# Kernel optimization log

Measured on AMD Instinct MI355X. Metric: run time of the kernel, lower is better.

## Reference

```python
import jax, jax.numpy as jnp
import numpy as np

INPUT_DIM = 256
OUTPUT_DIM = 512
NUM_KNOTS = 64
RANGE_KNOTS = (-1.0, 1.0)
DEGREE = 3
BATCH = 4096


def bspline_basis(x, knots, degree):
    """Cox-de Boor recursion. x: [B, I], knots: [K] (uniform, ascending).
    Returns basis values [B, I, K - degree - 1]."""
    xe = x[..., None]  # [B, I, 1]
    # degree-0: indicator of knot interval k, k = 0..K-2
    basis = ((xe >= knots[:-1]) & (xe < knots[1:])).astype(x.dtype)  # [B, I, K-1]
    for d in range(1, degree + 1):
        k = np.arange(knots.shape[0] - d - 1)
        left = (xe - knots[k]) / (knots[k + d] - knots[k]) * basis[..., :-1]
        right = (knots[k + d + 1] - xe) / (knots[k + d + 1] - knots[k + 1]) * basis[..., 1:]
        basis = left + right  # [B, I, K-d-1]
    return basis


def setup_inputs() -> dict:
    key = jax.random.key(0)
    kx, kb, ks = jax.random.split(key, 3)
    x = jax.random.uniform(kx, (BATCH, INPUT_DIM), dtype=jnp.float32)
    wb = jax.random.uniform(kb, (INPUT_DIM, OUTPUT_DIM), dtype=jnp.float32)
    ws = jax.random.uniform(ks, (INPUT_DIM, OUTPUT_DIM), dtype=jnp.float32)
    cps = jnp.ones((INPUT_DIM, NUM_KNOTS), dtype=jnp.float32)
    knots = jnp.asarray(np.linspace(RANGE_KNOTS[0], RANGE_KNOTS[1], NUM_KNOTS), dtype=jnp.float32)
    return {"x": x, "wb": wb, "ws": ws, "cps": cps, "knots": knots}


def reference(x, wb, ws, cps, knots):
    num_basis = NUM_KNOTS - DEGREE - 1
    basis = bspline_basis(x, knots, DEGREE)            # [B, I, num_basis]
    # per-input-dim spline value: sum_k cps[i, k] * B_k(x[b, i])
    spline = jnp.einsum('bik,ik->bi', basis, cps[:, :num_basis])  # [B, I]
    base = jax.nn.silu(x)                               # [B, I]
    # out[b, o] = sum_i wb[i, o] * silu(x[b, i]) + ws[i, o] * spline[b, i]
    out = base @ wb + spline @ ws                       # [B, O]
    return out
```

## Files before the change

kernel.cpp:

```cpp
#include <hip/hip_runtime.h>
#include <hip/hip_bf16.h>

#define BATCH    4096
#define IN_DIM   256
#define OUT_DIM  512
#define KDIM     512
#define NKNOTS   64
#define NBASIS   60

typedef __attribute__((ext_vector_type(8))) short bf16x8;
typedef __attribute__((ext_vector_type(4))) float f32x4;

__device__ __forceinline__ short f2bf(float f) {
    __hip_bfloat16 h = __float2bfloat16(f);
    return *reinterpret_cast<short*>(&h);
}

__global__ __launch_bounds__(256) void prep_a_kernel(
        const float* __restrict__ x, const float* __restrict__ cps,
        const float* __restrict__ knots, short* __restrict__ A) {
    int idx = blockIdx.x * 256 + threadIdx.x;
    int b = idx >> 8;
    int i = idx & (IN_DIM - 1);

    float xv = x[idx];
    float base = xv / (1.0f + __expf(-xv));

    float u = (xv + 1.0f) * 31.5f;
    int   j = (int)floorf(u);
    float spline = 0.0f;
    if (j >= 0 && j <= 62) {
        float t  = (xv - knots[j]) * 31.5f;
        float t2 = t * t, t3 = t2 * t;
        float omt = 1.0f - t;
        const float c6 = 1.0f / 6.0f;
        float w0 = omt * omt * omt * c6;
        float w1 = (3.0f*t3 - 6.0f*t2 + 4.0f) * c6;
        float w2 = (-3.0f*t3 + 3.0f*t2 + 3.0f*t + 1.0f) * c6;
        float w3 = t3 * c6;
        const float* cp = cps + i * NKNOTS;
        int k0 = j - 3;
        if (k0     >= 0 && k0     < NBASIS) spline += w0 * cp[k0];
        if (k0 + 1 >= 0 && k0 + 1 < NBASIS) spline += w1 * cp[k0 + 1];
        if (k0 + 2 >= 0 && k0 + 2 < NBASIS) spline += w2 * cp[k0 + 2];
        if (k0 + 3 >= 0 && k0 + 3 < NBASIS) spline += w3 * cp[k0 + 3];
    }

    A[b * KDIM + i]          = f2bf(base);
    A[b * KDIM + IN_DIM + i] = f2bf(spline);
}

__global__ __launch_bounds__(256) void prep_b_kernel(
        const float* __restrict__ wb, const float* __restrict__ ws,
        short* __restrict__ Bt) {
    int idx = blockIdx.x * 256 + threadIdx.x;
    int n = idx >> 9;
    int k = idx & (KDIM - 1);
    float v = (k < IN_DIM) ? wb[k * OUT_DIM + n] : ws[(k - IN_DIM) * OUT_DIM + n];
    Bt[idx] = f2bf(v);
}

#define BM 64
#define BN 64
#define BK 64
#define LDSS 72

__global__ __launch_bounds__(256) void gemm_kernel(
        const short* __restrict__ A, const short* __restrict__ Bt,
        float* __restrict__ C) {
    __shared__ __align__(16) short As[BM * LDSS];
    __shared__ __align__(16) short Bs[BN * LDSS];

    const int m0 = blockIdx.y * BM;
    const int n0 = blockIdx.x * BN;
    const int tid  = threadIdx.x;
    const int lane = tid & 63;
    const int wave = tid >> 6;
    const int wm = (wave & 1) * 32;
    const int wn = (wave >> 1) * 32;
    const int fr   = lane & 15;
    const int koff = (lane >> 4) * 8;

    f32x4 acc[2][2] = {};

    const int c1 = tid, c2 = tid + 256;
    const int r1 = c1 >> 3, o1 = (c1 & 7) * 8;
    const int r2 = c2 >> 3, o2 = (c2 & 7) * 8;

    for (int k0 = 0; k0 < KDIM; k0 += BK) {
        *(uint4*)&As[r1 * LDSS + o1] = *(const uint4*)&A[(m0 + r1) * KDIM + k0 + o1];
        *(uint4*)&As[r2 * LDSS + o2] = *(const uint4*)&A[(m0 + r2) * KDIM + k0 + o2];
        *(uint4*)&Bs[r1 * LDSS + o1] = *(const uint4*)&Bt[(n0 + r1) * KDIM + k0 + o1];
        *(uint4*)&Bs[r2 * LDSS + o2] = *(const uint4*)&Bt[(n0 + r2) * KDIM + k0 + o2];
        __syncthreads();

        #pragma unroll
        for (int kk = 0; kk < BK; kk += 32) {
            bf16x8 a0 = *(const bf16x8*)&As[(wm + fr)      * LDSS + kk + koff];
            bf16x8 a1 = *(const bf16x8*)&As[(wm + 16 + fr) * LDSS + kk + koff];
            bf16x8 b0 = *(const bf16x8*)&Bs[(wn + fr)      * LDSS + kk + koff];
            bf16x8 b1 = *(const bf16x8*)&Bs[(wn + 16 + fr) * LDSS + kk + koff];
            acc[0][0] = __builtin_amdgcn_mfma_f32_16x16x32_bf16(a0, b0, acc[0][0], 0, 0, 0);
            acc[0][1] = __builtin_amdgcn_mfma_f32_16x16x32_bf16(a0, b1, acc[0][1], 0, 0, 0);
            acc[1][0] = __builtin_amdgcn_mfma_f32_16x16x32_bf16(a1, b0, acc[1][0], 0, 0, 0);
            acc[1][1] = __builtin_amdgcn_mfma_f32_16x16x32_bf16(a1, b1, acc[1][1], 0, 0, 0);
        }
        __syncthreads();
    }

    const int rbase = (lane >> 4) * 4;
    #pragma unroll
    for (int mt = 0; mt < 2; ++mt) {
        #pragma unroll
        for (int nt = 0; nt < 2; ++nt) {
            #pragma unroll
            for (int r = 0; r < 4; ++r) {
                int row = m0 + wm + mt * 16 + rbase + r;
                int col = n0 + wn + nt * 16 + fr;
                C[row * OUT_DIM + col] = acc[mt][nt][r];
            }
        }
    }
}

extern "C" void kernel_launch(void* const* d_in, const int* in_sizes, int n_in,
                              void* d_out, int out_size, void* d_ws, size_t ws_size,
                              hipStream_t stream) {
    const float* x     = (const float*)d_in[0];
    const float* wb    = (const float*)d_in[1];
    const float* ws    = (const float*)d_in[2];
    const float* cps   = (const float*)d_in[3];
    const float* knots = (const float*)d_in[4];
    float* out = (float*)d_out;

    short* Abf = (short*)d_ws;
    short* Btb = (short*)((char*)d_ws + (size_t)BATCH * KDIM * 2);

    prep_a_kernel<<<BATCH * IN_DIM / 256, 256, 0, stream>>>(x, cps, knots, Abf);
    prep_b_kernel<<<OUT_DIM * KDIM / 256, 256, 0, stream>>>(wb, ws, Btb);

    dim3 grid(OUT_DIM / BN, BATCH / BM);
    gemm_kernel<<<grid, 256, 0, stream>>>(Abf, Btb, out);
}
```

Baseline: 84.39 us.

## Fuse prep kernels, tile-transpose weights, use direct global-to-LDS loads with XOR swizzle

Merges the two prep kernels into one launch. Activation blocks stage a transposed bf16 copy of the control points in LDS, and weight blocks transpose through a padded LDS tile so both reads and writes are coalesced. The GEMM now uses global_load_lds to write tiles straight into LDS, with an XOR swizzle in place of padding to avoid bank conflicts. The control points are rounded to bf16 before use, which adds a small precision loss, and the prep kernel now launches only 320 blocks.

New measurement: 84.81 us, median of 2. Within noise of the previous version (+0.5%).

```diff
diff --git a/kernel.cpp b/kernel.cpp
--- a/kernel.cpp
+++ b/kernel.cpp
@@ -15,91 +15,129 @@
     __hip_bfloat16 h = __float2bfloat16(f);
     return *reinterpret_cast<short*>(&h);
 }
-
-__global__ __launch_bounds__(256) void prep_a_kernel(
-        const float* __restrict__ x, const float* __restrict__ cps,
-        const float* __restrict__ knots, short* __restrict__ A) {
-    int idx = blockIdx.x * 256 + threadIdx.x;
-    int b = idx >> 8;
-    int i = idx & (IN_DIM - 1);
-
-    float xv = x[idx];
-    float base = xv / (1.0f + __expf(-xv));
-
-    float u = (xv + 1.0f) * 31.5f;
-    int   j = (int)floorf(u);
-    float spline = 0.0f;
-    if (j >= 0 && j <= 62) {
-        float t  = (xv - knots[j]) * 31.5f;
-        float t2 = t * t, t3 = t2 * t;
-        float omt = 1.0f - t;
-        const float c6 = 1.0f / 6.0f;
-        float w0 = omt * omt * omt * c6;
-        float w1 = (3.0f*t3 - 6.0f*t2 + 4.0f) * c6;
-        float w2 = (-3.0f*t3 + 3.0f*t2 + 3.0f*t + 1.0f) * c6;
-        float w3 = t3 * c6;
-        const float* cp = cps + i * NKNOTS;
-        int k0 = j - 3;
-        if (k0     >= 0 && k0     < NBASIS) spline += w0 * cp[k0];
-        if (k0 + 1 >= 0 && k0 + 1 < NBASIS) spline += w1 * cp[k0 + 1];
-        if (k0 + 2 >= 0 && k0 + 2 < NBASIS) spline += w2 * cp[k0 + 2];
-        if (k0 + 3 >= 0 && k0 + 3 < NBASIS) spline += w3 * cp[k0 + 3];
-    }
-
-    A[b * KDIM + i]          = f2bf(base);
-    A[b * KDIM + IN_DIM + i] = f2bf(spline);
+__device__ __forceinline__ float bf2f(short s) {
+    __hip_bfloat16 h = *reinterpret_cast<__hip_bfloat16*>(&s);
+    return __bfloat162float(h);
 }
 
-__global__ __launch_bounds__(256) void prep_b_kernel(
-        const float* __restrict__ wb, const float* __restrict__ ws,
-        short* __restrict__ Bt) {
-    int idx = blockIdx.x * 256 + threadIdx.x;
-    int n = idx >> 9;
-    int k = idx & (KDIM - 1);
-    float v = (k < IN_DIM) ? wb[k * OUT_DIM + n] : ws[(k - IN_DIM) * OUT_DIM + n];
-    Bt[idx] = f2bf(v);
+__global__ __launch_bounds__(256) void prep_kernel(
+        const float* __restrict__ x, const float* __restrict__ wb,
+        const float* __restrict__ ws, const float* __restrict__ cps,
+        const float* __restrict__ knots,
+        short* __restrict__ A, short* __restrict__ Bt) {
+    __shared__ short cpsT[NKNOTS * IN_DIM];
+    __shared__ float tile[64 * 65];
+
+    const int tid = threadIdx.x;
+    const int bid = blockIdx.x;
+
+    if (bid < 256) {
+        for (int k4 = 0; k4 < NKNOTS; k4 += 4) {
+            float4 v = *(const float4*)&cps[tid * NKNOTS + k4];
+            cpsT[(k4 + 0) * IN_DIM + tid] = f2bf(v.x);
+            cpsT[(k4 + 1) * IN_DIM + tid] = f2bf(v.y);
+            cpsT[(k4 + 2) * IN_DIM + tid] = f2bf(v.z);
+            cpsT[(k4 + 3) * IN_DIM + tid] = f2bf(v.w);
+        }
+        __syncthreads();
+
+        for (int it = 0; it < 16; ++it) {
+            int e = (bid * 16 + it) * 256 + tid;
+            int b = e >> 8;
+            int i = e & (IN_DIM - 1);
+
+            float xv = x[e];
+            float base = xv / (1.0f + __expf(-xv));
+
+            float u = (xv + 1.0f) * 31.5f;
+            int   j = (int)floorf(u);
+            float spline = 0.0f;
+            if (j >= 0 && j <= 62) {
+                float t  = (xv - knots[j]) * 31.5f;
+                float t2 = t * t, t3 = t2 * t;
+                float omt = 1.0f - t;
+                const float c6 = 1.0f / 6.0f;
+                float w0 = omt * omt * omt * c6;
+                float w1 = (3.0f*t3 - 6.0f*t2 + 4.0f) * c6;
+                float w2 = (-3.0f*t3 + 3.0f*t2 + 3.0f*t + 1.0f) * c6;
+                float w3 = t3 * c6;
+                int k0 = j - 3;
+                if (k0     >= 0 && k0     < NBASIS) spline += w0 * bf2f(cpsT[(k0    ) * IN_DIM + i]);
+                if (k0 + 1 >= 0 && k0 + 1 < NBASIS) spline += w1 * bf2f(cpsT[(k0 + 1) * IN_DIM + i]);
+                if (k0 + 2 >= 0 && k0 + 2 < NBASIS) spline += w2 * bf2f(cpsT[(k0 + 2) * IN_DIM + i]);
+                if (k0 + 3 >= 0 && k0 + 3 < NBASIS) spline += w3 * bf2f(cpsT[(k0 + 3) * IN_DIM + i]);
+            }
+            A[b * KDIM + i]          = f2bf(base);
+            A[b * KDIM + IN_DIM + i] = f2bf(spline);
+        }
+    } else {
+        int t = bid - 256;
+        const float* W = (t & 32) ? ws : wb;
+        int koffs = (t & 32) ? IN_DIM : 0;
+        int kb = ((t >> 3) & 3) * 64;
+        int nb = (t & 7) * 64;
+
+        for (int it = 0; it < 16; ++it) {
+            int f = it * 256 + tid;
+            int r = f >> 6, c = f & 63;
+            tile[r * 65 + c] = W[(kb + r) * OUT_DIM + nb + c];
+        }
+        __syncthreads();
+        for (int it = 0; it < 16; ++it) {
+            int f = it * 256 + tid;
+            int n = f >> 6, k = f & 63;
+            Bt[(nb + n) * KDIM + koffs + kb + k] = f2bf(tile[k * 65 + n]);
+        }
+    }
 }
 
 #define BM 64
 #define BN 64
 #define BK 64
-#define LDSS 72
+
+#define GLOAD_LDS16(g, l)                                                  \
+    __builtin_amdgcn_global_load_lds(                                      \
+        (const __attribute__((address_space(1))) void*)(g),                \
+        (__attribute__((address_space(3))) void*)(l), 16, 0, 0)
 
 __global__ __launch_bounds__(256) void gemm_kernel(
         const short* __restrict__ A, const short* __restrict__ Bt,
         float* __restrict__ C) {
-    __shared__ __align__(16) short As[BM * LDSS];
-    __shared__ __align__(16) short Bs[BN * LDSS];
+    __shared__ __align__(16) short As[BM * BK];
+    __shared__ __align__(16) short Bs[BN * BK];
 
-    const int m0 = blockIdx.y * BM;
-    const int n0 = blockIdx.x * BN;
     const int tid  = threadIdx.x;
     const int lane = tid & 63;
     const int wave = tid >> 6;
+    const int m0 = blockIdx.y * BM;
+    const int n0 = blockIdx.x * BN;
     const int wm = (wave & 1) * 32;
     const int wn = (wave >> 1) * 32;
-    const int fr   = lane & 15;
-    const int koff = (lane >> 4) * 8;
+    const int fr = lane & 15;
+    const int q  = lane >> 4;
+
+    const int lrow = lane >> 3;
+    const int c_sw = (lane & 7) ^ lrow;
+    const int ra0 = wave * 16 + lrow;
+    const int ra1 = wave * 16 + 8 + lrow;
 
     f32x4 acc[2][2] = {};
 
-    const int c1 = tid, c2 = tid + 256;
-    const int r1 = c1 >> 3, o1 = (c1 & 7) * 8;
-    const int r2 = c2 >> 3, o2 = (c2 & 7) * 8;
-
     for (int k0 = 0; k0 < KDIM; k0 += BK) {
-        *(uint4*)&As[r1 * LDSS + o1] = *(const uint4*)&A[(m0 + r1) * KDIM + k0 + o1];
-        *(uint4*)&As[r2 * LDSS + o2] = *(const uint4*)&A[(m0 + r2) * KDIM + k0 + o2];
-        *(uint4*)&Bs[r1 * LDSS + o1] = *(const uint4*)&Bt[(n0 + r1) * KDIM + k0 + o1];
-        *(uint4*)&Bs[r2 * LDSS + o2] = *(const uint4*)&Bt[(n0 + r2) * KDIM + k0 + o2];
+        GLOAD_LDS16(&A [(m0 + ra0) * KDIM + k0 + c_sw * 8], &As[(wave * 2    ) * 512]);
+        GLOAD_LDS16(&A [(m0 + ra1) * KDIM + k0 + c_sw * 8], &As[(wave * 2 + 1) * 512]);
+        GLOAD_LDS16(&Bt[(n0 + ra0) * KDIM + k0 + c_sw * 8], &Bs[(wave * 2    ) * 512]);
+        GLOAD_LDS16(&Bt[(n0 + ra1) * KDIM + k0 + c_sw * 8], &Bs[(wave * 2 + 1) * 512]);
         __syncthreads();
 
         #pragma unroll
-        for (int kk = 0; kk < BK; kk += 32) {
-            bf16x8 a0 = *(const bf16x8*)&As[(wm + fr)      * LDSS + kk + koff];
-            bf16x8 a1 = *(const bf16x8*)&As[(wm + 16 + fr) * LDSS + kk + koff];
-            bf16x8 b0 = *(const bf16x8*)&Bs[(wn + fr)      * LDSS + kk + koff];
-            bf16x8 b1 = *(const bf16x8*)&Bs[(wn + 16 + fr) * LDSS + kk + koff];
+        for (int kk = 0; kk < 2; ++kk) {
+            const int ck = kk * 4 + q;
+            const int sw = (ck ^ (fr & 7)) * 8;
+            bf16x8 a0 = *(const bf16x8*)&As[(wm + fr)      * BK + sw];
+            bf16x8 a1 = *(const bf16x8*)&As[(wm + 16 + fr) * BK + sw];
+            bf16x8 b0 = *(const bf16x8*)&Bs[(wn + fr)      * BK + sw];
+            bf16x8 b1 = *(const bf16x8*)&Bs[(wn + 16 + fr) * BK + sw];
             acc[0][0] = __builtin_amdgcn_mfma_f32_16x16x32_bf16(a0, b0, acc[0][0], 0, 0, 0);
             acc[0][1] = __builtin_amdgcn_mfma_f32_16x16x32_bf16(a0, b1, acc[0][1], 0, 0, 0);
             acc[1][0] = __builtin_amdgcn_mfma_f32_16x16x32_bf16(a1, b0, acc[1][0], 0, 0, 0);
@@ -108,7 +146,7 @@
         __syncthreads();
     }
 
-    const int rbase = (lane >> 4) * 4;
+    const int rbase = q * 4;
     #pragma unroll
     for (int mt = 0; mt < 2; ++mt) {
         #pragma unroll
@@ -136,8 +174,7 @@
     short* Abf = (short*)d_ws;
     short* Btb = (short*)((char*)d_ws + (size_t)BATCH * KDIM * 2);
 
-    prep_a_kernel<<<BATCH * IN_DIM / 256, 256, 0, stream>>>(x, cps, knots, Abf);
-    prep_b_kernel<<<OUT_DIM * KDIM / 256, 256, 0, stream>>>(wb, ws, Btb);
+    prep_kernel<<<320, 256, 0, stream>>>(x, wb, ws, cps, knots, Abf, Btb);
 
     dim3 grid(OUT_DIM / BN, BATCH / BM);
     gemm_kernel<<<grid, 256, 0, stream>>>(Abf, Btb, out);
```
